# Performance work log

Measured on AMD Instinct MI355X. Metric: run time of the kernel, lower is better.

## Reference

```python
import jax, jax.numpy as jnp
import numpy as np

B, N, C_IN = 4, 48, 32
HID = [32, 32]          # hidden_channel_list
NB = [32, 32]           # neighborhood_channels
C_OUT = 16
N_BASIS = 6             # equivariant 2->2 basis ops used by SnConv2


def _masked(t, mask):
    # zero out entries for padded nodes; mask: B,n,n,n bool, t: B,n,n,n,C
    return jnp.where(mask[..., None], t, jnp.zeros((), t.dtype))


def snconv2(t, W, b):
    """Sn-equivariant 2nd-order conv on dims (1,2); dim 3 rides along.
    t: B,i,j,m,C.  W: [6, C_in, C_out], one mixing matrix per basis op."""
    n = t.shape[1]
    tT = jnp.swapaxes(t, 1, 2)                       # transpose op
    diag = jnp.einsum('biimc->bimc', t)              # diagonal, B,i,m,C
    rows = t.sum(axis=2) / n                         # row sums,  B,i,m,C
    cols = t.sum(axis=1) / n                         # col sums,  B,j,m,C
    tot = t.sum(axis=(1, 2)) / (n * n)               # total sum, B,m,C
    # contract small features BEFORE broadcasting back to 2nd order
    out = (jnp.einsum('bijmc,cd->bijmd', t, W[0])
           + jnp.einsum('bijmc,cd->bijmd', tT, W[1])
           + jnp.einsum('bimc,cd->bimd', diag, W[2])[:, :, None]
           + jnp.einsum('bimc,cd->bimd', rows, W[3])[:, :, None]
           + jnp.einsum('bjmc,cd->bjmd', cols, W[4])[:, None]
           + jnp.einsum('bmc,cd->bmd', tot, W[5])[:, None, None]
           + b)
    return out


def localconv2(t, Wv, bv, Ww, bw, Wo, bo):
    """LocalConv2, product_type='elementwise': per-channel message passing
    along the node dims: z[b,i,j] = sum_k v[b,i,k] * w[b,k,j] / n."""
    n = t.shape[1]
    v = jnp.einsum('bijmc,cd->bijmd', t, Wv) + bv
    w = jnp.einsum('bijmc,cd->bijmd', t, Ww) + bw
    z = jnp.einsum('bikmc,bkjmc->bijmc', v, w) / n
    return jnp.einsum('bijmc,cd->bijmd', z, Wo) + bo


def setup_inputs() -> dict:
    key = jax.random.key(0)
    ks = jax.random.split(key, 24)
    x = jax.random.normal(ks[0], (B, N, C_IN), dtype=jnp.float32)
    # graphs of unequal size: per-graph node counts in [N//2, N]
    sizes = jax.random.randint(ks[1], (B,), N // 2, N + 1)
    node_valid = jnp.arange(N)[None, :] < sizes[:, None]            # B,n
    mask = (node_valid[:, :, None, None]
            & node_valid[:, None, :, None]
            & node_valid[:, None, None, :])                          # B,n,n,n
    s = 0.05
    inp = {'x': x, 'mask': mask}
    cin = C_IN
    for li, (nch, cout) in enumerate(zip(NB, HID)):
        inp[f'basic_W{li}'] = s * jax.random.normal(ks[2 + 8 * li], (N_BASIS, cin, cin), dtype=jnp.float32)
        inp[f'basic_b{li}'] = jnp.zeros((cin,), jnp.float32)
        inp[f'lv_W{li}'] = s * jax.random.normal(ks[3 + 8 * li], (cin, nch), dtype=jnp.float32)
        inp[f'lv_b{li}'] = jnp.zeros((nch,), jnp.float32)
        inp[f'lw_W{li}'] = s * jax.random.normal(ks[4 + 8 * li], (cin, nch), dtype=jnp.float32)
        inp[f'lw_b{li}'] = jnp.zeros((nch,), jnp.float32)
        inp[f'lo_W{li}'] = s * jax.random.normal(ks[5 + 8 * li], (nch, cout), dtype=jnp.float32)
        inp[f'lo_b{li}'] = jnp.zeros((cout,), jnp.float32)
        cin = cout
    inp['final_W'] = s * jax.random.normal(ks[20], (N_BASIS, cin, C_OUT), dtype=jnp.float32)
    inp['final_b'] = jnp.zeros((C_OUT,), jnp.float32)
    return inp


def reference(x, mask,
              basic_W0, basic_b0, lv_W0, lv_b0, lw_W0, lw_b0, lo_W0, lo_b0,
              basic_W1, basic_b1, lv_W1, lv_b1, lw_W1, lw_b1, lo_W1, lo_b1,
              final_W, final_b):
    # order-3 outer product T[b,i,j,k,c] = x[b,i,c]*x[b,j,c]*x[b,k,c]
    t = (x[:, :, None, None, :] * x[:, None, :, None, :]) * x[:, None, None, :, :]
    t = _masked(t, mask)
    layers = [(basic_W0, basic_b0, lv_W0, lv_b0, lw_W0, lw_b0, lo_W0, lo_b0),
              (basic_W1, basic_b1, lv_W1, lv_b1, lw_W1, lw_b1, lo_W1, lo_b1)]
    for bw_, bb_, vw, vb, ww, wb, ow, ob in layers:
        t = _masked(snconv2(t, bw_, bb_), mask)
        t = localconv2(t, vw, vb, ww, wb, ow, ob)
        t = jax.nn.relu(t)
        t = _masked(t, mask)
    out = _masked(snconv2(t, final_W, final_b), mask)
    return out
```

## Files before the change

kernel.cpp:

```cpp
#include <hip/hip_runtime.h>
#include <cstdint>


namespace {

constexpr int nB = 4, nN = 48, nC = 32;
constexpr int SJ_ = nN * nC;
constexpr int SI_ = nN * SJ_;
constexpr long SB_ = (long)nN * SI_;
constexpr int RP_ = 294912;
constexpr int CP_ = 294912;
constexpr int TP_ = 6144;

__device__ __forceinline__ void decodePos(int p, int& b, int& i, int& j, int& m) {
    m = p % nN; int r = p / nN;
    j = r % nN; r /= nN;
    i = r % nN; b = r / nN;
}

__global__ __launch_bounds__(256) void k_prepcomp(
    const float* __restrict__ x, const void* __restrict__ maskp,
    float* __restrict__ vm, float* __restrict__ S,
    const float* __restrict__ Wb0, const float* __restrict__ bb0,
    const float* __restrict__ Wv0, const float* __restrict__ Ww0,
    const float* __restrict__ Wb1, const float* __restrict__ bb1,
    const float* __restrict__ Wv1, const float* __restrict__ Ww1,
    float* __restrict__ cW, float* __restrict__ cb, float* __restrict__ cWs)
{
    __shared__ float Ws[1024];
    __shared__ float vmL[nB * nN];
    const int tid = threadIdx.x;

    if (blockIdx.x == 4) {
        const unsigned int w0 = *(const unsigned int*)maskp;
        const bool is_byte = (w0 == 0x01010101u);
        if (tid < nB * nN) {
            int b = tid / nN, i = tid % nN;
            long idx = ((long)(b * nN + i) * nN + i) * nN + i;
            int bit;
            if (is_byte) bit = (((const unsigned char*)maskp)[idx] != 0);
            else         bit = (((const int*)maskp)[idx] != 0);
            float f = bit ? 1.f : 0.f;
            vm[tid] = f; vmL[tid] = f;
        }
        __syncthreads();
        if (tid < nB * nC) {
            int b = tid >> 5, c = tid & 31;
            float s = 0.f;
            for (int j = 0; j < nN; ++j) s += x[(b * nN + j) * nC + c] * vmL[b * nN + j];
            S[tid] = s;
        }
        return;
    }

    const int blk = blockIdx.x;
    const float* Wb = (blk < 2) ? Wb0 : Wb1;
    const float* bb = (blk < 2) ? bb0 : bb1;
    const float* Wr = (blk == 0) ? Wv0 : (blk == 1) ? Ww0 : (blk == 2) ? Wv1 : Ww1;
    for (int q = tid; q < 1024; q += 256) Ws[q] = Wr[q];
    __syncthreads();
    for (int q = tid; q < 6144; q += 256) {
        const int d = q & 31;
        const float* row = Wb + (q >> 5) * 32;
        float s = 0.f;
        #pragma unroll
        for (int e = 0; e < 32; ++e) s = fmaf(row[e], Ws[e * 32 + d], s);
        cW[blk * 6144 + q] = s;
    }
    if (blk < 2) {
        for (int q = tid; q < 1024; q += 256) {
            const int d = q & 31; const int c = q >> 5;
            const float* r0 = Wb + c * 32;
            const float* r1 = Wb + 1024 + c * 32;
            float s = 0.f;
            #pragma unroll
            for (int e = 0; e < 32; ++e) s = fmaf(r0[e] + r1[e], Ws[e * 32 + d], s);
            cWs[blk * 1024 + q] = s;
        }
    }
    if (tid < 32) {
        float s = 0.f;
        #pragma unroll
        for (int e = 0; e < 32; ++e) s = fmaf(bb[e], Ws[e * 32 + tid], s);
        cb[blk * 32 + tid] = s;
    }
}

__global__ __launch_bounds__(256) void k_mix0(
    const float* __restrict__ x, const float* __restrict__ S,
    const float* __restrict__ Wb_a, const float* __restrict__ bias_a,
    float* __restrict__ dr_a, float* __restrict__ cc_a, float* __restrict__ tb_a,
    const float* __restrict__ Wb_b, const float* __restrict__ bias_b,
    float* __restrict__ dr_b, float* __restrict__ cc_b, float* __restrict__ tb_b)
{
    const int set = (blockIdx.x >= 36);
    const float* Wb   = set ? Wb_b   : Wb_a;
    const float* bias = set ? bias_b : bias_a;
    float* drp = set ? dr_b : dr_a;
    float* ccp = set ? cc_b : cc_a;
    float* tbp = set ? tb_b : tb_a;
    __shared__ float W2s[1024], W3s[1024], W4s[1024], W5s[1024], bs[32];
    const int tid = threadIdx.x;
    for (int q = tid; q < 1024; q += 256) {
        W2s[q] = Wb[2048 + q]; W3s[q] = Wb[3072 + q];
        W4s[q] = Wb[4096 + q]; W5s[q] = Wb[5120 + q];
    }
    if (tid < 32) bs[tid] = bias[tid];
    __syncthreads();
    const int id = (blockIdx.x - (set ? 36 : 0)) * 256 + tid;
    const int m = id % nN; int r = id / nN; const int i = r % nN; const int b = r / nN;
    float odr[32], occ[32];
    #pragma unroll
    for (int d = 0; d < 32; ++d) { odr[d] = 0.f; occ[d] = 0.f; }
    for (int c2 = 0; c2 < 32; ++c2) {
        float xi = x[(b * nN + i) * nC + c2];
        float xm = x[(b * nN + m) * nC + c2];
        float sc = S[b * nC + c2];
        float A = xi * xi * xm;
        float R = xi * xm * sc * (1.f / nN);
        #pragma unroll
        for (int d = 0; d < 32; ++d) {
            odr[d] = fmaf(A, W2s[c2 * 32 + d], fmaf(R, W3s[c2 * 32 + d], odr[d]));
            occ[d] = fmaf(R, W4s[c2 * 32 + d], occ[d]);
        }
    }
    #pragma unroll
    for (int d = 0; d < 32; d += 4) {
        *(float4*)(drp + (size_t)id * 32 + d) = make_float4(odr[d], odr[d+1], odr[d+2], odr[d+3]);
        *(float4*)(ccp + (size_t)id * 32 + d) = make_float4(occ[d], occ[d+1], occ[d+2], occ[d+3]);
    }
    if (i == 0) {
        float ot[32];
        #pragma unroll
        for (int d = 0; d < 32; ++d) ot[d] = bs[d];
        for (int c2 = 0; c2 < 32; ++c2) {
            float xm = x[(b * nN + m) * nC + c2];
            float sc = S[b * nC + c2];
            float Tc = xm * sc * sc * (1.f / (nN * nN));
            #pragma unroll
            for (int d = 0; d < 32; ++d) ot[d] = fmaf(Tc, W5s[c2 * 32 + d], ot[d]);
        }
        for (int d = 0; d < 32; d += 4)
            *(float4*)(tbp + (size_t)(b * nN + m) * 32 + d) = make_float4(ot[d], ot[d+1], ot[d+2], ot[d+3]);
    }
}

template <int DOUT>
__global__ __launch_bounds__(256) void k_mix(
    const float* __restrict__ dgp, const float* __restrict__ rw2,
    const float* __restrict__ cl2, const float* __restrict__ tt4,
    const float* __restrict__ Wb_a, const float* __restrict__ bias_a,
    float* __restrict__ dr_a, float* __restrict__ cc_a, float* __restrict__ tb_a,
    const float* __restrict__ Wb_b, const float* __restrict__ bias_b,
    float* __restrict__ dr_b, float* __restrict__ cc_b, float* __restrict__ tb_b)
{
    const int set = (blockIdx.x >= 36);
    const float* Wb   = set ? Wb_b   : Wb_a;
    const float* bias = set ? bias_b : bias_a;
    float* drp = set ? dr_b : dr_a;
    float* ccp = set ? cc_b : cc_a;
    float* tbp = set ? tb_b : tb_a;
    __shared__ float W2s[32 * DOUT], W3s[32 * DOUT], W4s[32 * DOUT], W5s[32 * DOUT], bs[DOUT];
    const int tid = threadIdx.x;
    for (int q = tid; q < 32 * DOUT; q += 256) {
        W2s[q] = Wb[2 * 32 * DOUT + q]; W3s[q] = Wb[3 * 32 * DOUT + q];
        W4s[q] = Wb[4 * 32 * DOUT + q]; W5s[q] = Wb[5 * 32 * DOUT + q];
    }
    if (tid < DOUT) bs[tid] = bias[tid];
    __syncthreads();
    const int id = (blockIdx.x - (set ? 36 : 0)) * 256 + tid;
    const int m = id % nN; int r = id / nN; const int i = r % nN; const int b = r / nN;
    float odr[DOUT], occ[DOUT];
    #pragma unroll
    for (int d = 0; d < DOUT; ++d) { odr[d] = 0.f; occ[d] = 0.f; }
    for (int c2 = 0; c2 < 32; ++c2) {
        size_t q = (size_t)id * 32 + c2;
        float dg = dgp[q];
        float rw = (rw2[q] + rw2[q + RP_]) * (1.f / nN);
        float cl = (cl2[q] + cl2[q + CP_]) * (1.f / nN);
        #pragma unroll
        for (int d = 0; d < DOUT; ++d) {
            odr[d] = fmaf(dg, W2s[c2 * DOUT + d], fmaf(rw, W3s[c2 * DOUT + d], odr[d]));
            occ[d] = fmaf(cl, W4s[c2 * DOUT + d], occ[d]);
        }
    }
    #pragma unroll
    for (int d = 0; d < DOUT; d += 4) {
        *(float4*)(drp + (size_t)id * DOUT + d) = make_float4(odr[d], odr[d+1], odr[d+2], odr[d+3]);
        *(float4*)(ccp + (size_t)id * DOUT + d) = make_float4(occ[d], occ[d+1], occ[d+2], occ[d+3]);
    }
    if (i == 0) {
        float ot[DOUT];
        #pragma unroll
        for (int d = 0; d < DOUT; ++d) ot[d] = bs[d];
        for (int c2 = 0; c2 < 32; ++c2) {
            size_t q = (size_t)(b * nN + m) * 32 + c2;
            float tv = (tt4[q] + tt4[q + TP_] + tt4[q + 2 * TP_] + tt4[q + 3 * TP_])
                       * (1.f / (nN * nN));
            #pragma unroll
            for (int d = 0; d < DOUT; ++d) ot[d] = fmaf(tv, W5s[c2 * DOUT + d], ot[d]);
        }
        for (int d = 0; d < DOUT; d += 4)
            *(float4*)(tbp + (size_t)(b * nN + m) * DOUT + d) = make_float4(ot[d], ot[d+1], ot[d+2], ot[d+3]);
    }
}

#define FMA4(ar, tv, w4)                       \
    ar[0] = fmaf(tv, w4.x, ar[0]);             \
    ar[1] = fmaf(tv, w4.y, ar[1]);             \
    ar[2] = fmaf(tv, w4.z, ar[2]);             \
    ar[3] = fmaf(tv, w4.w, ar[3]);

template <int MODE>
__global__ __launch_bounds__(256) void k_vw(
    const float* __restrict__ src, const float* __restrict__ vm,
    const float* __restrict__ drv, const float* __restrict__ ccv, const float* __restrict__ tbv,
    const float* __restrict__ drw, const float* __restrict__ ccw, const float* __restrict__ tbw,
    const float* __restrict__ Wv2, const float* __restrict__ Ww2,
    const float* __restrict__ bv, const float* __restrict__ bw,
    float* __restrict__ vout, float* __restrict__ wout)
{
    constexpr int CH = 64;
    constexpr int CS = CH * 34;
    constexpr int BUF = (MODE == 0) ? CS : 2 * CS;
    __shared__ float sT[2][BUF];
    __shared__ float wL[(MODE == 0) ? 2048 : 4096];
    const int tid = threadIdx.x;

    {
        float4* wl4 = (float4*)wL;
        for (int q = tid; q < 512; q += 256) wl4[q] = ((const float4*)Wv2)[q];
        if (MODE == 1)
            for (int q = tid; q < 512; q += 256) wl4[512 + q] = ((const float4*)Ww2)[q];
    }

    const int base0 = blockIdx.x * 9 * CH;
    float4 rA0, rA1, rB0, rB1;

    auto loadChunk = [&](int k) {
        const int cb = base0 + k * CH;
        {   const int q = tid; const int pl = q >> 3, cq = q & 7;
            const int p = cb + pl;
            if (MODE == 0) {
                int b, i, j, m; decodePos(p, b, i, j, m);
                float4 xi = *(const float4*)(src + (size_t)(b * nN + i) * nC + cq * 4);
                float4 xj = *(const float4*)(src + (size_t)(b * nN + j) * nC + cq * 4);
                float4 xm = *(const float4*)(src + (size_t)(b * nN + m) * nC + cq * 4);
                rA0.x = xi.x * xj.x * xm.x; rA0.y = xi.y * xj.y * xm.y;
                rA0.z = xi.z * xj.z * xm.z; rA0.w = xi.w * xj.w * xm.w;
            } else {
                rA0 = *(const float4*)(src + (size_t)p * nC + cq * 4);
                int b, i, j, m; decodePos(p, b, i, j, m);
                long pT = ((long)(b * nN + j) * nN + i) * nN + m;
                rB0 = *(const float4*)(src + pT * nC + cq * 4);
            }
        }
        {   const int q = 256 + tid; const int pl = q >> 3, cq = q & 7;
            const int p = cb + pl;
            if (MODE == 0) {
                int b, i, j, m; decodePos(p, b, i, j, m);
                float4 xi = *(const float4*)(src + (size_t)(b * nN + i) * nC + cq * 4);
                float4 xj = *(const float4*)(src + (size_t)(b * nN + j) * nC + cq * 4);
                float4 xm = *(const float4*)(src + (size_t)(b * nN + m) * nC + cq * 4);
                rA1.x = xi.x * xj.x * xm.x; rA1.y = xi.y * xj.y * xm.y;
                rA1.z = xi.z * xj.z * xm.z; rA1.w = xi.w * xj.w * xm.w;
            } else {
                rA1 = *(const float4*)(src + (size_t)p * nC + cq * 4);
                int b, i, j, m; decodePos(p, b, i, j, m);
                long pT = ((long)(b * nN + j) * nN + i) * nN + m;
                rB1 = *(const float4*)(src + pT * nC + cq * 4);
            }
        }
    };
    auto writeChunk = [&](int buf) {
        {   const int q = tid; const int o = (q >> 3) * 34 + (q & 7) * 4;
            sT[buf][o + 0] = rA0.x; sT[buf][o + 1] = rA0.y;
            sT[buf][o + 2] = rA0.z; sT[buf][o + 3] = rA0.w;
            if (MODE == 1) {
                sT[buf][CS + o + 0] = rB0.x; sT[buf][CS + o + 1] = rB0.y;
                sT[buf][CS + o + 2] = rB0.z; sT[buf][CS + o + 3] = rB0.w;
            }
        }
        {   const int q = 256 + tid; const int o = (q >> 3) * 34 + (q & 7) * 4;
            sT[buf][o + 0] = rA1.x; sT[buf][o + 1] = rA1.y;
            sT[buf][o + 2] = rA1.z; sT[buf][o + 3] = rA1.w;
            if (MODE == 1) {
                sT[buf][CS + o + 0] = rB1.x; sT[buf][CS + o + 1] = rB1.y;
                sT[buf][CS + o + 2] = rB1.z; sT[buf][CS + o + 3] = rB1.w;
            }
        }
    };

    loadChunk(0);
    writeChunk(0);
    __syncthreads();

    const int pt = tid >> 3, dq = tid & 7;
    const int p0 = pt * 2, d0 = dq * 4;

    for (int k = 0; k < 9; ++k) {
        const int cur = k & 1;
        if (k < 8) loadChunk(k + 1);
        __builtin_amdgcn_sched_barrier(0);

        float accv[2][4], accw[2][4];
        #pragma unroll
        for (int l = 0; l < 2; ++l)
            #pragma unroll
            for (int d = 0; d < 4; ++d) { accv[l][d] = 0.f; accw[l][d] = 0.f; }

        const float* sp = sT[cur];
        #pragma unroll
        for (int cp = 0; cp < 16; ++cp) {
            float2 t0 = *(const float2*)(sp + (p0 + 0) * 34 + cp * 2);
            float2 t1 = *(const float2*)(sp + (p0 + 1) * 34 + cp * 2);
            const int c0 = cp * 2, c1 = cp * 2 + 1;
            const float* wwb = (MODE == 0) ? (wL + 1024) : (wL + 2048);
            float4 wv0 = *(const float4*)(wL + c0 * nC + d0);
            float4 wv1 = *(const float4*)(wL + c1 * nC + d0);
            float4 ww0 = *(const float4*)(wwb + c0 * nC + d0);
            float4 ww1 = *(const float4*)(wwb + c1 * nC + d0);
            FMA4(accv[0], t0.x, wv0); FMA4(accv[1], t1.x, wv0);
            FMA4(accv[0], t0.y, wv1); FMA4(accv[1], t1.y, wv1);
            FMA4(accw[0], t0.x, ww0); FMA4(accw[1], t1.x, ww0);
            FMA4(accw[0], t0.y, ww1); FMA4(accw[1], t1.y, ww1);
        }
        if (MODE == 1) {
            #pragma unroll
            for (int cp = 0; cp < 16; ++cp) {
                float2 t0 = *(const float2*)(sp + CS + (p0 + 0) * 34 + cp * 2);
                float2 t1 = *(const float2*)(sp + CS + (p0 + 1) * 34 + cp * 2);
                const int c0 = cp * 2, c1 = cp * 2 + 1;
                float4 wv0 = *(const float4*)(wL + 1024 + c0 * nC + d0);
                float4 wv1 = *(const float4*)(wL + 1024 + c1 * nC + d0);
                float4 ww0 = *(const float4*)(wL + 3072 + c0 * nC + d0);
                float4 ww1 = *(const float4*)(wL + 3072 + c1 * nC + d0);
                FMA4(accv[0], t0.x, wv0); FMA4(accv[1], t1.x, wv0);
                FMA4(accv[0], t0.y, wv1); FMA4(accv[1], t1.y, wv1);
                FMA4(accw[0], t0.x, ww0); FMA4(accw[1], t1.x, ww0);
                FMA4(accw[0], t0.y, ww1); FMA4(accw[1], t1.y, ww1);
            }
        }

        const int cb = base0 + k * CH;
        {
            float4 b4 = *(const float4*)(bv + d0);
            #pragma unroll
            for (int l = 0; l < 2; ++l) {
                int p = cb + p0 + l;
                int b, i, j, m; decodePos(p, b, i, j, m);
                float4 d4 = *(const float4*)(drv + (size_t)((b * nN + i) * nN + m) * nC + d0);
                float4 c4 = *(const float4*)(ccv + (size_t)((b * nN + j) * nN + m) * nC + d0);
                float4 t4 = *(const float4*)(tbv + (size_t)(b * nN + m) * nC + d0);
                float mk = vm[b * nN + i] * vm[b * nN + j] * vm[b * nN + m];
                float4 o4;
                o4.x = (accv[l][0] + d4.x + c4.x + t4.x) * mk + b4.x;
                o4.y = (accv[l][1] + d4.y + c4.y + t4.y) * mk + b4.y;
                o4.z = (accv[l][2] + d4.z + c4.z + t4.z) * mk + b4.z;
                o4.w = (accv[l][3] + d4.w + c4.w + t4.w) * mk + b4.w;
                *(float4*)(vout + (size_t)p * nC + d0) = o4;
            }
        }
        {
            float4 b4 = *(const float4*)(bw + d0);
            #pragma unroll
            for (int l = 0; l < 2; ++l) {
                int p = cb + p0 + l;
                int b, i, j, m; decodePos(p, b, i, j, m);
                float4 d4 = *(const float4*)(drw + (size_t)((b * nN + i) * nN + m) * nC + d0);
                float4 c4 = *(const float4*)(ccw + (size_t)((b * nN + j) * nN + m) * nC + d0);
                float4 t4 = *(const float4*)(tbw + (size_t)(b * nN + m) * nC + d0);
                float mk = vm[b * nN + i] * vm[b * nN + j] * vm[b * nN + m];
                float4 o4;
                o4.x = (accw[l][0] + d4.x + c4.x + t4.x) * mk + b4.x;
                o4.y = (accw[l][1] + d4.y + c4.y + t4.y) * mk + b4.y;
                o4.z = (accw[l][2] + d4.z + c4.z + t4.z) * mk + b4.z;
                o4.w = (accw[l][3] + d4.w + c4.w + t4.w) * mk + b4.w;
                *(float4*)(wout + (size_t)p * nC + d0) = o4;
            }
        }

        if (k < 8) {
            writeChunk((k + 1) & 1);
            __syncthreads();
        }
    }
}

__global__ __launch_bounds__(256, 3) void k_z(
    const float* __restrict__ v, const float* __restrict__ w,
    const float* __restrict__ Wo, const float* __restrict__ bo,
    const float* __restrict__ vm, float* __restrict__ tout,
    float* __restrict__ rows2, float* __restrict__ cols2,
    float* __restrict__ diag_, float* __restrict__ tot4)
{
    __shared__ float lds[12912];
    float* Vt = lds;
    float* Wt = lds + 6456;
    constexpr int ZS = 34;
    constexpr int ZWO = 9792;
    constexpr int TOT0 = 10816;
    const int tid = threadIdx.x;
    const int blk = blockIdx.x;
    const int tl = blk & 3; const int bm = blk >> 2;
    const int it = tl >> 1, jt = tl & 1;
    const int b = bm / nN, m = bm % nN;
    const int c = tid & 31;
    const int g = tid >> 5;
    const int i3 = g >> 1, j2 = g & 1;
    const int il0 = i3 * 6, jl0 = j2 * 12;
    const size_t posbase = (size_t)b * SB_ + (size_t)m * nC;

    float acc[6][12];
    #pragma unroll
    for (int l = 0; l < 6; ++l)
        #pragma unroll
        for (int u = 0; u < 12; ++u) acc[l][u] = 0.f;

    for (int kc = 0; kc < 6; ++kc) {
        if (kc) __syncthreads();
        #pragma unroll
        for (int rr = 0; rr < 6; ++rr) {
            int q = rr * 256 + tid; int pos = q >> 3, cq = q & 7;
            int ii = pos >> 3, kk = pos & 7;
            float4 a = *(const float4*)(v + posbase + (size_t)(it * 24 + ii) * SI_
                                          + (size_t)(kc * 8 + kk) * SJ_ + cq * 4);
            float* dst = Vt + kk * 807 + (cq * 4) * 25 + ii;
            dst[0] = a.x; dst[25] = a.y; dst[50] = a.z; dst[75] = a.w;
        }
        #pragma unroll
        for (int rr = 0; rr < 6; ++rr) {
            int q = rr * 256 + tid; int pos = q >> 3, cq = q & 7;
            int kk = pos / 24, jj = pos - kk * 24;
            float4 a = *(const float4*)(w + posbase + (size_t)(kc * 8 + kk) * SI_
                                          + (size_t)(jt * 24 + jj) * SJ_ + cq * 4);
            float* dst = Wt + kk * 807 + (cq * 4) * 25 + jj;
            dst[0] = a.x; dst[25] = a.y; dst[50] = a.z; dst[75] = a.w;
        }
        __syncthreads();
        #pragma unroll
        for (int kk = 0; kk < 8; ++kk) {
            float vf[6], wf[12];
            #pragma unroll
            for (int l = 0; l < 6; ++l) vf[l] = Vt[kk * 807 + c * 25 + il0 + l];
            #pragma unroll
            for (int u = 0; u < 12; ++u) wf[u] = Wt[kk * 807 + c * 25 + jl0 + u];
            #pragma unroll
            for (int l = 0; l < 6; ++l)
                #pragma unroll
                for (int u = 0; u < 12; ++u)
                    acc[l][u] = fmaf(vf[l], wf[u], acc[l][u]);
        }
    }
    __syncthreads();

    #pragma unroll
    for (int e = 0; e < 4; ++e)
        lds[ZWO + e * 256 + tid] = Wo[e * 256 + tid] * (1.f / nN);

    const int ptE = tid >> 3, dqE = tid & 7, d0 = dqE * 4;
    const float4 b4 = *(const float4*)(bo + d0);
    const float vmm = vm[b * nN + m];
    float colacc[3] = {0.f, 0.f, 0.f};
    float totacc = 0.f;

    for (int h = 0; h < 2; ++h) {
        if (h) __syncthreads();
        if ((i3 >> 1) == h) {
            int r0 = il0 - 12 * h;
            #pragma unroll
            for (int l = 0; l < 6; ++l)
                #pragma unroll
                for (int u = 0; u < 12; ++u)
                    lds[((r0 + l) * 24 + jl0 + u) * ZS + c] = acc[l][u];
        }
        __syncthreads();

        float oac[9][4];
        #pragma unroll
        for (int u = 0; u < 9; ++u)
            #pragma unroll
            for (int d = 0; d < 4; ++d) oac[u][d] = 0.f;
        #pragma unroll
        for (int c2 = 0; c2 < 32; ++c2) {
            float4 wo4 = *(const float4*)(lds + ZWO + c2 * 32 + d0);
            float zv[9];
            #pragma unroll
            for (int u = 0; u < 9; ++u) zv[u] = lds[(ptE * 9 + u) * ZS + c2];
            #pragma unroll
            for (int u = 0; u < 9; ++u) {
                oac[u][0] = fmaf(zv[u], wo4.x, oac[u][0]);
                oac[u][1] = fmaf(zv[u], wo4.y, oac[u][1]);
                oac[u][2] = fmaf(zv[u], wo4.z, oac[u][2]);
                oac[u][3] = fmaf(zv[u], wo4.w, oac[u][3]);
            }
        }
        __syncthreads();

        #pragma unroll
        for (int u = 0; u < 9; ++u) {
            int p = ptE * 9 + u;
            int rl = p / 24, jl = p - rl * 24;
            int gi = it * 24 + 12 * h + rl, gj = jt * 24 + jl;
            float mk = vm[b * nN + gi] * vm[b * nN + gj] * vmm;
            float4 o4;
            o4.x = fmaxf(oac[u][0] + b4.x, 0.f) * mk;
            o4.y = fmaxf(oac[u][1] + b4.y, 0.f) * mk;
            o4.z = fmaxf(oac[u][2] + b4.z, 0.f) * mk;
            o4.w = fmaxf(oac[u][3] + b4.w, 0.f) * mk;
            *(float4*)(tout + posbase + (size_t)gi * SI_ + (size_t)gj * SJ_ + d0) = o4;
            *(float2*)(lds + p * ZS + d0) = make_float2(o4.x, o4.y);
            *(float2*)(lds + p * ZS + d0 + 2) = make_float2(o4.z, o4.w);
        }
        __syncthreads();

        for (int rd = 0; rd < 2; ++rd) {
            int task = rd * 256 + tid;
            if (task < 384) {
                int i_r = task >> 5, c_r = task & 31;
                float rsum = 0.f;
                #pragma unroll
                for (int jl = 0; jl < 24; ++jl) rsum += lds[(i_r * 24 + jl) * ZS + c_r];
                int gi = it * 24 + 12 * h + i_r;
                rows2[(size_t)jt * RP_ + ((size_t)(b * nN + gi) * nN + m) * nC + c_r] = rsum;
                totacc += rsum;
                if (it == jt)
                    diag_[((size_t)(b * nN + gi) * nN + m) * nC + c_r] =
                        lds[(i_r * 24 + (12 * h + i_r)) * ZS + c_r];
            }
        }
        #pragma unroll
        for (int rr = 0; rr < 3; ++rr) {
            int task = rr * 256 + tid;
            int jl = task >> 5, c_c = task & 31;
            float csum = 0.f;
            #pragma unroll
            for (int il = 0; il < 12; ++il) csum += lds[(il * 24 + jl) * ZS + c_c];
            colacc[rr] += csum;
        }
    }

    #pragma unroll
    for (int rr = 0; rr < 3; ++rr) {
        int task = rr * 256 + tid;
        int jl = task >> 5, c_c = task & 31;
        cols2[(size_t)it * CP_ + ((size_t)(b * nN + jt * 24 + jl) * nN + m) * nC + c_c] = colacc[rr];
    }
    lds[TOT0 + g * 32 + c] = totacc;
    __syncthreads();
    if (tid < 32) {
        float s = 0.f;
        #pragma unroll
        for (int gg = 0; gg < 8; ++gg) s += lds[TOT0 + gg * 32 + tid];
        tot4[(size_t)(it * 2 + jt) * TP_ + (size_t)(b * nN + m) * nC + tid] = s;
    }
}

__global__ __launch_bounds__(256) void k_final(
    const float* __restrict__ t, const float* __restrict__ vm,
    const float* __restrict__ drp, const float* __restrict__ ccp, const float* __restrict__ tbp,
    const float* __restrict__ W0, const float* __restrict__ W1,
    float* __restrict__ out)
{
    constexpr int CH = 64, CS = CH * 34;
    __shared__ float sT[2][2 * CS];
    __shared__ float wL[1024];
    const int tid = threadIdx.x;

    {
        float4* wl4 = (float4*)wL;
        for (int q = tid; q < 128; q += 256) wl4[q] = ((const float4*)W0)[q];
        for (int q = tid; q < 128; q += 256) wl4[128 + q] = ((const float4*)W1)[q];
    }

    const int base0 = blockIdx.x * 9 * CH;
    float4 rA0, rA1, rB0, rB1;

    auto loadChunk = [&](int k) {
        const int cb = base0 + k * CH;
        {   const int q = tid; const int pl = q >> 3, cq = q & 7;
            const int p = cb + pl;
            rA0 = *(const float4*)(t + (size_t)p * nC + cq * 4);
            int b, i, j, m; decodePos(p, b, i, j, m);
            long pT = ((long)(b * nN + j) * nN + i) * nN + m;
            rB0 = *(const float4*)(t + pT * nC + cq * 4);
        }
        {   const int q = 256 + tid; const int pl = q >> 3, cq = q & 7;
            const int p = cb + pl;
            rA1 = *(const float4*)(t + (size_t)p * nC + cq * 4);
            int b, i, j, m; decodePos(p, b, i, j, m);
            long pT = ((long)(b * nN + j) * nN + i) * nN + m;
            rB1 = *(const float4*)(t + pT * nC + cq * 4);
        }
    };
    auto writeChunk = [&](int buf) {
        {   const int q = tid; const int o = (q >> 3) * 34 + (q & 7) * 4;
            sT[buf][o + 0] = rA0.x; sT[buf][o + 1] = rA0.y;
            sT[buf][o + 2] = rA0.z; sT[buf][o + 3] = rA0.w;
            sT[buf][CS + o + 0] = rB0.x; sT[buf][CS + o + 1] = rB0.y;
            sT[buf][CS + o + 2] = rB0.z; sT[buf][CS + o + 3] = rB0.w;
        }
        {   const int q = 256 + tid; const int o = (q >> 3) * 34 + (q & 7) * 4;
            sT[buf][o + 0] = rA1.x; sT[buf][o + 1] = rA1.y;
            sT[buf][o + 2] = rA1.z; sT[buf][o + 3] = rA1.w;
            sT[buf][CS + o + 0] = rB1.x; sT[buf][CS + o + 1] = rB1.y;
            sT[buf][CS + o + 2] = rB1.z; sT[buf][CS + o + 3] = rB1.w;
        }
    };

    loadChunk(0);
    writeChunk(0);
    __syncthreads();

    const int pt = tid >> 3, dq = tid & 7;
    const int p0 = pt * 2, d0 = dq * 2;

    for (int k = 0; k < 9; ++k) {
        const int cur = k & 1;
        if (k < 8) loadChunk(k + 1);
        __builtin_amdgcn_sched_barrier(0);

        float acc[2][2];
        acc[0][0] = 0.f; acc[0][1] = 0.f; acc[1][0] = 0.f; acc[1][1] = 0.f;
        const float* sp = sT[cur];
        #pragma unroll
        for (int cp = 0; cp < 16; ++cp) {
            float2 t0 = *(const float2*)(sp + (p0 + 0) * 34 + cp * 2);
            float2 t1 = *(const float2*)(sp + (p0 + 1) * 34 + cp * 2);
            const int c0 = cp * 2, c1 = cp * 2 + 1;
            float2 w0 = *(const float2*)(wL + c0 * 16 + d0);
            float2 w1 = *(const float2*)(wL + c1 * 16 + d0);
            acc[0][0] = fmaf(t0.x, w0.x, acc[0][0]); acc[0][1] = fmaf(t0.x, w0.y, acc[0][1]);
            acc[1][0] = fmaf(t1.x, w0.x, acc[1][0]); acc[1][1] = fmaf(t1.x, w0.y, acc[1][1]);
            acc[0][0] = fmaf(t0.y, w1.x, acc[0][0]); acc[0][1] = fmaf(t0.y, w1.y, acc[0][1]);
            acc[1][0] = fmaf(t1.y, w1.x, acc[1][0]); acc[1][1] = fmaf(t1.y, w1.y, acc[1][1]);
        }
        #pragma unroll
        for (int cp = 0; cp < 16; ++cp) {
            float2 t0 = *(const float2*)(sp + CS + (p0 + 0) * 34 + cp * 2);
            float2 t1 = *(const float2*)(sp + CS + (p0 + 1) * 34 + cp * 2);
            const int c0 = cp * 2, c1 = cp * 2 + 1;
            float2 w0 = *(const float2*)(wL + 512 + c0 * 16 + d0);
            float2 w1 = *(const float2*)(wL + 512 + c1 * 16 + d0);
            acc[0][0] = fmaf(t0.x, w0.x, acc[0][0]); acc[0][1] = fmaf(t0.x, w0.y, acc[0][1]);
            acc[1][0] = fmaf(t1.x, w0.x, acc[1][0]); acc[1][1] = fmaf(t1.x, w0.y, acc[1][1]);
            acc[0][0] = fmaf(t0.y, w1.x, acc[0][0]); acc[0][1] = fmaf(t0.y, w1.y, acc[0][1]);
            acc[1][0] = fmaf(t1.y, w1.x, acc[1][0]); acc[1][1] = fmaf(t1.y, w1.y, acc[1][1]);
        }

        const int cb = base0 + k * CH;
        #pragma unroll
        for (int l = 0; l < 2; ++l) {
            int p = cb + p0 + l;
            int b, i, j, m; decodePos(p, b, i, j, m);
            float2 d2 = *(const float2*)(drp + (size_t)((b * nN + i) * nN + m) * 16 + d0);
            float2 cc2 = *(const float2*)(ccp + (size_t)((b * nN + j) * nN + m) * 16 + d0);
            float2 tb2 = *(const float2*)(tbp + (size_t)(b * nN + m) * 16 + d0);
            float mk = vm[b * nN + i] * vm[b * nN + j] * vm[b * nN + m];
            float2 o2;
            o2.x = (acc[l][0] + d2.x + cc2.x + tb2.x) * mk;
            o2.y = (acc[l][1] + d2.y + cc2.y + tb2.y) * mk;
            *(float2*)(out + (size_t)p * 16 + d0) = o2;
        }

        if (k < 8) {
            writeChunk((k + 1) & 1);
            __syncthreads();
        }
    }
}

}

extern "C" void kernel_launch(void* const* d_in, const int* in_sizes, int n_in,
                              void* d_out, int out_size, void* d_ws, size_t ws_size,
                              hipStream_t stream)
{
    (void)in_sizes; (void)n_in; (void)out_size; (void)ws_size;
    const float* x    = (const float*)d_in[0];
    const void*  mask = d_in[1];
    const float* bW0  = (const float*)d_in[2];
    const float* bb0  = (const float*)d_in[3];
    const float* lvW0 = (const float*)d_in[4];
    const float* lvb0 = (const float*)d_in[5];
    const float* lwW0 = (const float*)d_in[6];
    const float* lwb0 = (const float*)d_in[7];
    const float* loW0 = (const float*)d_in[8];
    const float* lob0 = (const float*)d_in[9];
    const float* bW1  = (const float*)d_in[10];
    const float* bb1  = (const float*)d_in[11];
    const float* lvW1 = (const float*)d_in[12];
    const float* lvb1 = (const float*)d_in[13];
    const float* lwW1 = (const float*)d_in[14];
    const float* lwb1 = (const float*)d_in[15];
    const float* loW1 = (const float*)d_in[16];
    const float* lob1 = (const float*)d_in[17];
    const float* fW   = (const float*)d_in[18];
    const float* fb   = (const float*)d_in[19];

    float* ws  = (float*)d_ws;
    float* t     = ws;
    float* v     = ws + 14155776L;
    float* w     = ws + 28311552L;
    float* rows2 = ws + 42467328L;
    float* cols2 = rows2 + 2 * 294912;
    float* diag  = cols2 + 2 * 294912;
    float* tot4  = diag + 294912;
    float* drv   = tot4 + 4 * 6144;
    float* ccv   = drv + 294912;
    float* tbv   = ccv + 294912;
    float* drw   = tbv + 6144;
    float* ccw   = drw + 294912;
    float* tbw   = ccw + 294912;
    float* cW    = tbw + 6144;
    float* cb    = cW + 4 * 6144;
    float* cWs   = cb + 128;
    float* S     = cWs + 2048;
    float* vm    = S + 128;
    float* out   = (float*)d_out;

    k_prepcomp<<<5, 256, 0, stream>>>(x, mask, vm, S,
                                      bW0, bb0, lvW0, lwW0,
                                      bW1, bb1, lvW1, lwW1, cW, cb, cWs);

    k_mix0<<<72, 256, 0, stream>>>(x, S,
                                   cW + 0,    cb + 0,  drv, ccv, tbv,
                                   cW + 6144, cb + 32, drw, ccw, tbw);
    k_vw<0><<<768, 256, 0, stream>>>(x, vm, drv, ccv, tbv, drw, ccw, tbw,
                                     cWs,
                                     cWs,
                                     lvb0, lwb0, v, w);
    k_z<<<768, 256, 0, stream>>>(v, w, loW0, lob0, vm, t, rows2, cols2, diag, tot4);

    k_mix<32><<<72, 256, 0, stream>>>(diag, rows2, cols2, tot4,
                                      cW + 12288, cb + 64, drv, ccv, tbv,
                                      cW + 18432, cb + 96, drw, ccw, tbw);
    k_vw<1><<<768, 256, 0, stream>>>(t, vm, drv, ccv, tbv, drw, ccw, tbw,
                                     cW + 12288,
                                     cW + 18432,
                                     lvb1, lwb1, v, w);
    k_z<<<768, 256, 0, stream>>>(v, w, loW1, lob1, vm, t, rows2, cols2, diag, tot4);

    k_mix<16><<<36, 256, 0, stream>>>(diag, rows2, cols2, tot4,
                                      fW, fb, drv, ccv, tbv,
                                      fW, fb, drv, ccv, tbv);
    k_final<<<768, 256, 0, stream>>>(t, vm, drv, ccv, tbv, fW, fW + 512, out);
}
```

Before: 497.7 us.

## Double-buffer k_z LDS tiles with register prefetch and remap blocks per XCD

The k_z contraction loop now streams the k dimension in 12 chunks of 4 instead of 6 chunks of 8. Each chunk is split into two LDS halves used as a double buffer, and the next chunk's global loads are issued into registers before computing on the current one. This hides global load latency behind the FMA work and removes one barrier per chunk. Block indices are also remapped so that consecutive (b,m) slices land on the same XCD, which should improve L2 sharing between the four tiles of one slice. The cost is extra registers for the prefetched float4s, which may pressure occupancy under the 3-blocks-per-CU bound.

New measurement: 462.4 us. 7.1% less time.

```diff
diff --git a/kernel.cpp b/kernel.cpp
--- a/kernel.cpp
+++ b/kernel.cpp
@@ -395,14 +395,14 @@
     float* __restrict__ diag_, float* __restrict__ tot4)
 {
     __shared__ float lds[12912];
-    float* Vt = lds;
-    float* Wt = lds + 6456;
+    constexpr int HB = 6456;
     constexpr int ZS = 34;
     constexpr int ZWO = 9792;
     constexpr int TOT0 = 10816;
     const int tid = threadIdx.x;
-    const int blk = blockIdx.x;
-    const int tl = blk & 3; const int bm = blk >> 2;
+    const int idb = blockIdx.x;
+    const int xcd = idb & 7; const int qq = idb >> 3;
+    const int tl = qq & 3; const int bm = (qq >> 2) * 8 + xcd;
     const int it = tl >> 1, jt = tl & 1;
     const int b = bm / nN, m = bm % nN;
     const int c = tid & 31;
@@ -411,35 +411,67 @@
     const int il0 = i3 * 6, jl0 = j2 * 12;
     const size_t posbase = (size_t)b * SB_ + (size_t)m * nC;
 
+    const int q0 = tid, q1 = 256 + tid, q2 = 512 + tid;
+    const int pV0 = q0 >> 3, pV1 = q1 >> 3, pV2 = q2 >> 3;
+    const int cq0 = (q0 & 7) * 4, cq1 = (q1 & 7) * 4, cq2 = (q2 & 7) * 4;
+    const int iiV0 = pV0 >> 2, kkV0 = pV0 & 3;
+    const int iiV1 = pV1 >> 2, kkV1 = pV1 & 3;
+    const int iiV2 = pV2 >> 2, kkV2 = pV2 & 3;
+    const int kkW0 = pV0 / 24, jjW0 = pV0 - kkW0 * 24;
+    const int kkW1 = pV1 / 24, jjW1 = pV1 - kkW1 * 24;
+    const int kkW2 = pV2 / 24, jjW2 = pV2 - kkW2 * 24;
+    const float* vs0 = v + posbase + (size_t)(it * 24 + iiV0) * SI_ + (size_t)kkV0 * SJ_ + cq0;
+    const float* vs1 = v + posbase + (size_t)(it * 24 + iiV1) * SI_ + (size_t)kkV1 * SJ_ + cq1;
+    const float* vs2 = v + posbase + (size_t)(it * 24 + iiV2) * SI_ + (size_t)kkV2 * SJ_ + cq2;
+    const float* ws0 = w + posbase + (size_t)kkW0 * SI_ + (size_t)(jt * 24 + jjW0) * SJ_ + cq0;
+    const float* ws1 = w + posbase + (size_t)kkW1 * SI_ + (size_t)(jt * 24 + jjW1) * SJ_ + cq1;
+    const float* ws2 = w + posbase + (size_t)kkW2 * SI_ + (size_t)(jt * 24 + jjW2) * SJ_ + cq2;
+    const int dV0 = kkV0 * 807 + cq0 * 25 + iiV0;
+    const int dV1 = kkV1 * 807 + cq1 * 25 + iiV1;
+    const int dV2 = kkV2 * 807 + cq2 * 25 + iiV2;
+    const int dW0 = 3228 + kkW0 * 807 + cq0 * 25 + jjW0;
+    const int dW1 = 3228 + kkW1 * 807 + cq1 * 25 + jjW1;
+    const int dW2 = 3228 + kkW2 * 807 + cq2 * 25 + jjW2;
+
+    float4 rv0, rv1, rv2, rw0, rw1, rw2;
+
+    auto loadChunk = [&](int ch) {
+        const size_t ov = (size_t)ch * 4 * SJ_;
+        const size_t ow = (size_t)ch * 4 * SI_;
+        rv0 = *(const float4*)(vs0 + ov);
+        rv1 = *(const float4*)(vs1 + ov);
+        rv2 = *(const float4*)(vs2 + ov);
+        rw0 = *(const float4*)(ws0 + ow);
+        rw1 = *(const float4*)(ws1 + ow);
+        rw2 = *(const float4*)(ws2 + ow);
+    };
+    auto writeChunk = [&](int bufi) {
+        float* bp = lds + bufi * HB;
+        bp[dV0] = rv0.x; bp[dV0 + 25] = rv0.y; bp[dV0 + 50] = rv0.z; bp[dV0 + 75] = rv0.w;
+        bp[dV1] = rv1.x; bp[dV1 + 25] = rv1.y; bp[dV1 + 50] = rv1.z; bp[dV1 + 75] = rv1.w;
+        bp[dV2] = rv2.x; bp[dV2 + 25] = rv2.y; bp[dV2 + 50] = rv2.z; bp[dV2 + 75] = rv2.w;
+        bp[dW0] = rw0.x; bp[dW0 + 25] = rw0.y; bp[dW0 + 50] = rw0.z; bp[dW0 + 75] = rw0.w;
+        bp[dW1] = rw1.x; bp[dW1 + 25] = rw1.y; bp[dW1 + 50] = rw1.z; bp[dW1 + 75] = rw1.w;
+        bp[dW2] = rw2.x; bp[dW2 + 25] = rw2.y; bp[dW2 + 50] = rw2.z; bp[dW2 + 75] = rw2.w;
+    };
+
     float acc[6][12];
     #pragma unroll
     for (int l = 0; l < 6; ++l)
         #pragma unroll
         for (int u = 0; u < 12; ++u) acc[l][u] = 0.f;
 
-    for (int kc = 0; kc < 6; ++kc) {
-        if (kc) __syncthreads();
-        #pragma unroll
-        for (int rr = 0; rr < 6; ++rr) {
-            int q = rr * 256 + tid; int pos = q >> 3, cq = q & 7;
-            int ii = pos >> 3, kk = pos & 7;
-            float4 a = *(const float4*)(v + posbase + (size_t)(it * 24 + ii) * SI_
-                                          + (size_t)(kc * 8 + kk) * SJ_ + cq * 4);
-            float* dst = Vt + kk * 807 + (cq * 4) * 25 + ii;
-            dst[0] = a.x; dst[25] = a.y; dst[50] = a.z; dst[75] = a.w;
-        }
-        #pragma unroll
-        for (int rr = 0; rr < 6; ++rr) {
-            int q = rr * 256 + tid; int pos = q >> 3, cq = q & 7;
-            int kk = pos / 24, jj = pos - kk * 24;
-            float4 a = *(const float4*)(w + posbase + (size_t)(kc * 8 + kk) * SI_
-                                          + (size_t)(jt * 24 + jj) * SJ_ + cq * 4);
-            float* dst = Wt + kk * 807 + (cq * 4) * 25 + jj;
-            dst[0] = a.x; dst[25] = a.y; dst[50] = a.z; dst[75] = a.w;
-        }
-        __syncthreads();
-        #pragma unroll
-        for (int kk = 0; kk < 8; ++kk) {
+    loadChunk(0);
+    writeChunk(0);
+    __syncthreads();
+
+    for (int ch = 0; ch < 12; ++ch) {
+        if (ch < 11) loadChunk(ch + 1);
+        __builtin_amdgcn_sched_barrier(0);
+        const float* Vt = lds + (ch & 1) * HB;
+        const float* Wt = Vt + 3228;
+        #pragma unroll
+        for (int kk = 0; kk < 4; ++kk) {
             float vf[6], wf[12];
             #pragma unroll
             for (int l = 0; l < 6; ++l) vf[l] = Vt[kk * 807 + c * 25 + il0 + l];
@@ -450,6 +482,10 @@
                 #pragma unroll
                 for (int u = 0; u < 12; ++u)
                     acc[l][u] = fmaf(vf[l], wf[u], acc[l][u]);
+        }
+        if (ch < 11) {
+            writeChunk((ch + 1) & 1);
+            __syncthreads();
         }
     }
     __syncthreads();
```
